# Performance work log

Hardware: AMD Instinct MI355X
Metric: run time of the kernel (lower is better)

## Reference

```python
import jax, jax.numpy as jnp
import numpy as np

N0, N1, N2 = 100000, 50000, 25000
E0, E1 = 400000, 200000
H1, D1 = 4, 64   # layer0: 4 heads x 64
H2, D2 = 1, 64   # layer1: 1 head  x 64
SLOPE = 0.2      # DGL GATConv leaky_relu negative_slope


def gat_conv(h_src, h_dst, src, dst, W, attn_l, attn_r, bias, n_dst, heads, d):
    # linear projection (shared between src and dst, as in DGL GATConv)
    f_src = (h_src @ W).reshape(-1, heads, d)   # (N_src, H, D)
    f_dst = (h_dst @ W).reshape(-1, heads, d)   # (N_dst, H, D)
    el = jnp.einsum('nhd,hd->nh', f_src, attn_l)  # (N_src, H)
    er = jnp.einsum('nhd,hd->nh', f_dst, attn_r)  # (N_dst, H)
    e = jax.nn.leaky_relu(el[src] + er[dst], SLOPE)  # (E, H)
    # edge-softmax over incoming edges of each dst node (numerically stable)
    m = jax.ops.segment_max(e, dst, num_segments=n_dst)      # (N_dst, H)
    ee = jnp.exp(e - m[dst])
    s = jax.ops.segment_sum(ee, dst, num_segments=n_dst)
    alpha = ee / s[dst]                                      # (E, H)
    msg = f_src[src] * alpha[:, :, None]                     # (E, H, D)
    out = jax.ops.segment_sum(msg, dst, num_segments=n_dst)  # (N_dst, H, D)
    return out + bias.reshape(1, heads, d)


def setup_inputs() -> dict:
    key = jax.random.key(0)
    ks = jax.random.split(key, 12)
    return {
        'x': jax.random.normal(ks[0], (N0, 256), jnp.float32),
        'e0_src': jax.random.randint(ks[1], (E0,), 0, N0, jnp.int32),
        'e0_dst': jax.random.randint(ks[2], (E0,), 0, N1, jnp.int32),
        'e1_src': jax.random.randint(ks[3], (E1,), 0, N1, jnp.int32),
        'e1_dst': jax.random.randint(ks[4], (E1,), 0, N2, jnp.int32),
        'W1': jax.random.normal(ks[5], (256, H1 * D1), jnp.float32) * 0.06,
        'al1': jax.random.normal(ks[6], (H1, D1), jnp.float32) * 0.1,
        'ar1': jax.random.normal(ks[7], (H1, D1), jnp.float32) * 0.1,
        'b1': jnp.zeros((H1 * D1,), jnp.float32),
        'W2': jax.random.normal(ks[8], (H1 * D1, H2 * D2), jnp.float32) * 0.06,
        'al2': jax.random.normal(ks[9], (H2, D2), jnp.float32) * 0.1,
        'ar2': jax.random.normal(ks[10], (H2, D2), jnp.float32) * 0.1,
        'b2': jnp.zeros((H2 * D2,), jnp.float32),
    }


def reference(x, e0_src, e0_dst, e1_src, e1_dst,
              W1, al1, ar1, b1, W2, al2, ar2, b2):
    # layer 0: block 100k src -> 50k dst; dst nodes are a prefix of src nodes
    h = gat_conv(x, x[:N1], e0_src, e0_dst, W1, al1, ar1, b1, N1, H1, D1)
    h = jax.nn.relu(h).reshape(N1, H1 * D1)   # activation + flatten(1); dropout is identity at eval
    # layer 1 (final): single head, no activation, flatten
    h = gat_conv(h, h[:N2], e1_src, e1_dst, W2, al2, ar2, b2, N2, H2, D2)
    return h.reshape(N2, H2 * D2)
```

## Files before the change

kernel.cpp:

```cpp
#include <hip/hip_runtime.h>
#include <cstddef>
#include <cstdint>

constexpr int cN0 = 100000, cN1 = 50000, cN2 = 25000;
constexpr int cE0 = 400000, cE1 = 200000;
constexpr float SLOPE = 0.2f;

typedef short short8  __attribute__((ext_vector_type(8)));
typedef short short4v __attribute__((ext_vector_type(4)));
typedef float f32x4   __attribute__((ext_vector_type(4)));

__device__ __forceinline__ unsigned short f2bf(float x) {
    union { float f; uint32_t u; } c; c.f = x;
    uint32_t u = c.u + 0x7FFFu + ((c.u >> 16) & 1u);
    return (unsigned short)(u >> 16);
}
__device__ __forceinline__ float bf2f(uint32_t u) {
    union { uint32_t u; float f; } c; c.u = u << 16; return c.f;
}
__device__ __forceinline__ float lrelu(float x) { return x >= 0.f ? x : SLOPE * x; }


__global__ void hist2_kernel(const int* __restrict__ d0, const int* __restrict__ d1,
                             int* __restrict__ cnt0, int* __restrict__ cnt1) {
    int i = blockIdx.x * blockDim.x + threadIdx.x;
    if (i < cE0) atomicAdd(&cnt0[d0[i]], 1);
    int j = i - cE0;
    if (j >= 0 && j < cE1) atomicAdd(&cnt1[d1[j]], 1);
}

__global__ __launch_bounds__(256) void chunk_sum2_kernel(const int* __restrict__ cnt0, int n0,
                                                         const int* __restrict__ cnt1, int n1,
                                                         int* __restrict__ bsum0, int* __restrict__ bsum1,
                                                         int nblk1) {
    const int* cnt = blockIdx.y ? cnt1 : cnt0;
    int n = blockIdx.y ? n1 : n0;
    int* bsum = blockIdx.y ? bsum1 : bsum0;
    if (blockIdx.y && (int)blockIdx.x >= nblk1) return;
    int i = blockIdx.x * 256 + threadIdx.x;
    int v = (i < n) ? cnt[i] : 0;
    #pragma unroll
    for (int o = 32; o; o >>= 1) v += __shfl_xor(v, o);
    __shared__ int ws[4];
    if ((threadIdx.x & 63) == 0) ws[threadIdx.x >> 6] = v;
    __syncthreads();
    if (threadIdx.x == 0) bsum[blockIdx.x] = ws[0] + ws[1] + ws[2] + ws[3];
}

__device__ __forceinline__ int block_exscan(int v, int& total) {
    int lane = threadIdx.x & 63, w = threadIdx.x >> 6;
    int x = v;
    #pragma unroll
    for (int o = 1; o < 64; o <<= 1) { int t = __shfl_up(x, o); if (lane >= o) x += t; }
    __shared__ int ws[4];
    if (lane == 63) ws[w] = x;
    __syncthreads();
    int add = 0;
    #pragma unroll
    for (int i = 0; i < 4; ++i) if (i < w) add += ws[i];
    total = ws[0] + ws[1] + ws[2] + ws[3];
    return add + x - v;
}

__global__ __launch_bounds__(256) void top_scan2_kernel(const int* __restrict__ bsum0, int nblk0,
                                                        const int* __restrict__ bsum1, int nblk1,
                                                        int* __restrict__ boff0, int* __restrict__ boff1,
                                                        int* __restrict__ tot0, int* __restrict__ tot1) {
    int i = threadIdx.x;
    int tot;
    int v = (i < nblk0) ? bsum0[i] : 0;
    int e = block_exscan(v, tot);
    if (i < nblk0) boff0[i] = e;
    if (i == 0) *tot0 = tot;
    __syncthreads();
    v = (i < nblk1) ? bsum1[i] : 0;
    e = block_exscan(v, tot);
    if (i < nblk1) boff1[i] = e;
    if (i == 0) *tot1 = tot;
}

__global__ __launch_bounds__(256) void chunk_scan2_kernel(const int* __restrict__ cnt0, int n0,
                                                          const int* __restrict__ cnt1, int n1,
                                                          const int* __restrict__ boff0, const int* __restrict__ boff1,
                                                          int* __restrict__ offs0, int* __restrict__ cursor0,
                                                          int* __restrict__ offs1, int* __restrict__ cursor1,
                                                          int nblk1) {
    const int* cnt = blockIdx.y ? cnt1 : cnt0;
    const int* boff = blockIdx.y ? boff1 : boff0;
    int* offs = blockIdx.y ? offs1 : offs0;
    int* cursor = blockIdx.y ? cursor1 : cursor0;
    int n = blockIdx.y ? n1 : n0;
    if (blockIdx.y && (int)blockIdx.x >= nblk1) return;
    int i = blockIdx.x * 256 + threadIdx.x;
    int v = (i < n) ? cnt[i] : 0;
    int tot; int e = block_exscan(v, tot) + boff[blockIdx.x];
    if (i < n) { offs[i] = e; cursor[i] = e; }
}

__global__ void scatter2_kernel(const int* __restrict__ s0, const int* __restrict__ d0,
                                const int* __restrict__ s1, const int* __restrict__ d1,
                                int* __restrict__ cursor0, int* __restrict__ srcidx0,
                                int* __restrict__ cursor1, int* __restrict__ srcidx1) {
    int i = blockIdx.x * blockDim.x + threadIdx.x;
    if (i < cE0) { int p = atomicAdd(&cursor0[d0[i]], 1); srcidx0[p] = s0[i]; }
    int j = i - cE0;
    if (j >= 0 && j < cE1) { int p = atomicAdd(&cursor1[d1[j]], 1); srcidx1[p] = s1[j]; }
}

__global__ __launch_bounds__(256) void bf16_transpose2_kernel(const float* __restrict__ W1,
                                                              const float* __restrict__ W2,
                                                              short* __restrict__ bt1,
                                                              short* __restrict__ bt2) {
    int i = blockIdx.x * 256 + threadIdx.x;
    if (i < 256 * 256) {
        int k = i >> 8, n = i & 255;
        bt1[(size_t)n * 256 + k] = (short)f2bf(W1[i]);
    } else {
        int j = i - 256 * 256;
        if (j < 256 * 64) {
            int k = j >> 6, n = j & 63;
            bt2[(size_t)n * 256 + k] = (short)f2bf(W2[j]);
        }
    }
}

__global__ __launch_bounds__(512, 4) void gemm0_deep(
    const float* __restrict__ A, const short* __restrict__ BT,
    unsigned short* __restrict__ C,
    const float* __restrict__ al, const float* __restrict__ ar,
    float* __restrict__ el, float* __restrict__ er,
    int M, int K, int erN)
{
    constexpr int BM = 128, BN = 256, BK = 32;
    constexpr int PITCH = BK + 8;
    constexpr int WR = 2, WC = 4;
    constexpr int MI = BM / WR / 16;
    constexpr int NI = BN / WC / 16;
    constexpr int nh = 4;

    __shared__ short As[2][BM * PITCH];
    __shared__ short Bs[2][BN * PITCH];

    const int tid = threadIdx.x;
    const int w = tid >> 6;
    const int lane = tid & 63;
    const int ln = lane & 15;
    const int kg = lane >> 4;
    const int wr = w / WC;
    const int wc = w % WC;
    const int m0 = blockIdx.x * BM;
    const int N = BN;

    f32x4 acc[MI][NI];
    #pragma unroll
    for (int mi = 0; mi < MI; ++mi)
        #pragma unroll
        for (int ni = 0; ni < NI; ++ni)
            #pragma unroll
            for (int j = 0; j < 4; ++j) acc[mi][ni][j] = 0.f;

    float4 areg[2];
    short8 breg[2];

    auto loadA = [&](int k0) {
        #pragma unroll
        for (int p = 0; p < 2; ++p) {
            int slot = tid + p * 512;
            int r = slot >> 3;
            int kq = (slot & 7) * 4;
            int gr = m0 + r;
            float4 v = make_float4(0.f, 0.f, 0.f, 0.f);
            if (gr < M) v = *(const float4*)&A[(size_t)gr * K + k0 + kq];
            areg[p] = v;
        }
    };
    auto loadB = [&](int k0) {
        #pragma unroll
        for (int p = 0; p < 2; ++p) {
            int slot = tid + p * 512;
            int r = slot >> 2;
            int kq = (slot & 3) * 8;
            breg[p] = *(const short8*)&BT[(size_t)r * K + k0 + kq];
        }
    };
    auto writeLDS = [&](int c) {
        #pragma unroll
        for (int p = 0; p < 2; ++p) {
            int slot = tid + p * 512;
            int r = slot >> 3;
            int kq = (slot & 7) * 4;
            short4v s;
            s[0] = (short)f2bf(areg[p].x); s[1] = (short)f2bf(areg[p].y);
            s[2] = (short)f2bf(areg[p].z); s[3] = (short)f2bf(areg[p].w);
            *(short4v*)&As[c][r * PITCH + kq] = s;
        }
        #pragma unroll
        for (int p = 0; p < 2; ++p) {
            int slot = tid + p * 512;
            int r = slot >> 2;
            int kq = (slot & 3) * 8;
            *(short8*)&Bs[c][r * PITCH + kq] = breg[p];
        }
    };

    loadA(0); loadB(0);
    writeLDS(0);
    __syncthreads();

    const int T = K / BK;
    int cur = 0;
    for (int t = 0; t < T; ++t) {
        if (t + 1 < T) { loadA((t + 1) * BK); loadB((t + 1) * BK); }
        short8 af[MI];
        #pragma unroll
        for (int mi = 0; mi < MI; ++mi)
            af[mi] = *(const short8*)&As[cur][(wr * MI * 16 + mi * 16 + ln) * PITCH + kg * 8];
        #pragma unroll
        for (int ni = 0; ni < NI; ++ni) {
            short8 bf = *(const short8*)&Bs[cur][(wc * NI * 16 + ni * 16 + ln) * PITCH + kg * 8];
            #pragma unroll
            for (int mi = 0; mi < MI; ++mi)
                acc[mi][ni] = __builtin_amdgcn_mfma_f32_16x16x32_bf16(af[mi], bf, acc[mi][ni], 0, 0, 0);
        }
        if (t + 1 < T) { writeLDS(cur ^ 1); cur ^= 1; }
        __syncthreads();
    }

    const int h = wc;
    float alv[NI], arv[NI];
    #pragma unroll
    for (int ni = 0; ni < NI; ++ni) {
        alv[ni] = al[h * 64 + ni * 16 + ln];
        arv[ni] = ar[h * 64 + ni * 16 + ln];
    }
    #pragma unroll
    for (int mi = 0; mi < MI; ++mi) {
        float pl[4] = {0, 0, 0, 0}, pr[4] = {0, 0, 0, 0};
        #pragma unroll
        for (int ni = 0; ni < NI; ++ni)
            #pragma unroll
            for (int j = 0; j < 4; ++j) {
                float v = acc[mi][ni][j];
                pl[j] += v * alv[ni];
                pr[j] += v * arv[ni];
            }
        #pragma unroll
        for (int j = 0; j < 4; ++j)
            #pragma unroll
            for (int o = 1; o < 16; o <<= 1) {
                pl[j] += __shfl_xor(pl[j], o);
                pr[j] += __shfl_xor(pr[j], o);
            }
        #pragma unroll
        for (int j = 0; j < 4; ++j) {
            int row = m0 + wr * MI * 16 + mi * 16 + kg * 4 + j;
            if (row < M) {
                #pragma unroll
                for (int ni = 0; ni < NI; ++ni)
                    C[(size_t)row * N + wc * 64 + ni * 16 + ln] = f2bf(acc[mi][ni][j]);
                if (ln == 0) {
                    el[row * nh + h] = pl[j];
                    if (row < erN) er[row * nh + h] = pr[j];
                }
            }
        }
    }
}

template<int BM, int BN, int WR, int WC>
__global__ __launch_bounds__(256) void gemm_bf16_fused(
    const unsigned short* __restrict__ A, const short* __restrict__ BT,
    unsigned short* __restrict__ C,
    const float* __restrict__ al, const float* __restrict__ ar,
    float* __restrict__ el, float* __restrict__ er,
    int M, int K, int nh, int erN)
{
    constexpr int BK = 32;
    constexpr int PITCH = BK + 8;
    constexpr int MI = BM / WR / 16;
    constexpr int NI = BN / WC / 16;
    constexpr int AITB = BM * 4 / 256;
    constexpr int BIT  = BN * 4 / 256;

    __shared__ short As[BM * PITCH];
    __shared__ short Bs[BN * PITCH];

    const int tid = threadIdx.x;
    const int w = tid >> 6;
    const int lane = tid & 63;
    const int ln = lane & 15;
    const int kg = lane >> 4;
    const int wr = w / WC;
    const int wc = w % WC;
    const int m0 = blockIdx.x * BM;
    const int n0 = blockIdx.y * BN;
    const int N = nh * 64;

    f32x4 acc[MI][NI];
    #pragma unroll
    for (int mi = 0; mi < MI; ++mi)
        #pragma unroll
        for (int ni = 0; ni < NI; ++ni)
            #pragma unroll
            for (int j = 0; j < 4; ++j) acc[mi][ni][j] = 0.f;

    short8 aregb[AITB];
    short8 breg[BIT];

    auto loadA = [&](int k0) {
        #pragma unroll
        for (int p = 0; p < AITB; ++p) {
            int slot = tid + p * 256;
            int r = slot >> 2;
            int kq = (slot & 3) * 8;
            int gr = m0 + r;
            short8 v = {};
            if (gr < M) v = *(const short8*)&A[(size_t)gr * K + k0 + kq];
            aregb[p] = v;
        }
    };
    auto loadB = [&](int k0) {
        #pragma unroll
        for (int p = 0; p < BIT; ++p) {
            int slot = tid + p * 256;
            int r = slot >> 2;
            int kq = (slot & 3) * 8;
            breg[p] = *(const short8*)&BT[(size_t)(n0 + r) * K + k0 + kq];
        }
    };
    auto writeLDS = [&]() {
        #pragma unroll
        for (int p = 0; p < AITB; ++p) {
            int slot = tid + p * 256;
            int r = slot >> 2;
            int kq = (slot & 3) * 8;
            *(short8*)&As[r * PITCH + kq] = aregb[p];
        }
        #pragma unroll
        for (int p = 0; p < BIT; ++p) {
            int slot = tid + p * 256;
            int r = slot >> 2;
            int kq = (slot & 3) * 8;
            *(short8*)&Bs[r * PITCH + kq] = breg[p];
        }
    };

    loadA(0); loadB(0);
    const int T = K / BK;
    for (int t = 0; t < T; ++t) {
        writeLDS();
        __syncthreads();
        if (t + 1 < T) { loadA((t + 1) * BK); loadB((t + 1) * BK); }
        short8 af[MI], bf[NI];
        #pragma unroll
        for (int mi = 0; mi < MI; ++mi)
            af[mi] = *(const short8*)&As[(wr * MI * 16 + mi * 16 + ln) * PITCH + kg * 8];
        #pragma unroll
        for (int ni = 0; ni < NI; ++ni)
            bf[ni] = *(const short8*)&Bs[(wc * NI * 16 + ni * 16 + ln) * PITCH + kg * 8];
        #pragma unroll
        for (int mi = 0; mi < MI; ++mi)
            #pragma unroll
            for (int ni = 0; ni < NI; ++ni)
                acc[mi][ni] = __builtin_amdgcn_mfma_f32_16x16x32_bf16(af[mi], bf[ni], acc[mi][ni], 0, 0, 0);
        __syncthreads();
    }

    const int h = (n0 + wc * NI * 16) >> 6;
    float alv[NI], arv[NI];
    #pragma unroll
    for (int ni = 0; ni < NI; ++ni) {
        alv[ni] = al[h * 64 + ni * 16 + ln];
        arv[ni] = ar[h * 64 + ni * 16 + ln];
    }
    #pragma unroll
    for (int mi = 0; mi < MI; ++mi) {
        float pl[4] = {0, 0, 0, 0}, pr[4] = {0, 0, 0, 0};
        #pragma unroll
        for (int ni = 0; ni < NI; ++ni)
            #pragma unroll
            for (int j = 0; j < 4; ++j) {
                float v = acc[mi][ni][j];
                pl[j] += v * alv[ni];
                pr[j] += v * arv[ni];
            }
        #pragma unroll
        for (int j = 0; j < 4; ++j)
            #pragma unroll
            for (int o = 1; o < 16; o <<= 1) {
                pl[j] += __shfl_xor(pl[j], o);
                pr[j] += __shfl_xor(pr[j], o);
            }
        #pragma unroll
        for (int j = 0; j < 4; ++j) {
            int row = m0 + wr * MI * 16 + mi * 16 + kg * 4 + j;
            if (row < M) {
                #pragma unroll
                for (int ni = 0; ni < NI; ++ni)
                    C[(size_t)row * N + n0 + wc * NI * 16 + ni * 16 + ln] = f2bf(acc[mi][ni][j]);
                if (ln == 0) {
                    el[row * nh + h] = pl[j];
                    if (row < erN) er[row * nh + h] = pr[j];
                }
            }
        }
    }
}


__global__ __launch_bounds__(256) void agg0_kernel(const int* __restrict__ offs,
                                                   const int* __restrict__ srcidx,
                                                   const float* __restrict__ el,
                                                   const float* __restrict__ er,
                                                   const unsigned short* __restrict__ fb,
                                                   const float* __restrict__ bias,
                                                   unsigned short* __restrict__ h1b) {
    int w = threadIdx.x >> 6, lane = threadIdx.x & 63;
    int n = blockIdx.x * 4 + w;
    if (n >= cN1) return;
    int beg = offs[n], end = offs[n + 1];

    int h4 = lane & 3, sub = lane >> 2;
    float erA = er[n * 4 + h4];
    float m = -1e30f, s = 0.f;
    for (int i = beg + sub; i < end; i += 16) {
        int sv = srcidx[i];
        float e = lrelu(el[sv * 4 + h4] + erA);
        if (e > m) { s = s * __expf(m - e) + 1.f; m = e; }
        else s += __expf(e - m);
    }
    #pragma unroll
    for (int o = 4; o < 64; o <<= 1) {
        float m2 = __shfl_xor(m, o), s2 = __shfl_xor(s, o);
        float M = fmaxf(m, m2);
        s = s * __expf(m - M) + s2 * __expf(m2 - M);
        m = M;
    }
    float inv = (s > 0.f) ? 1.f / s : 0.f;

    int half = lane >> 5, lcol = lane & 31;
    int hB = lcol >> 3;
    float mB = __shfl(m, hB);
    float invB = __shfl(inv, hB);
    float erB = __shfl(erA, hB);

    float a[8] = {};
    for (int i = beg + half; i < end; i += 2) {
        int sv = srcidx[i];
        float e = lrelu(el[sv * 4 + hB] + erB);
        float p = __expf(e - mB) * invB;
        uint4 v = *(const uint4*)&fb[(size_t)sv * 256 + lcol * 8];
        a[0] = fmaf(bf2f(v.x & 0xffffu), p, a[0]);
        a[1] = fmaf(bf2f(v.x >> 16),     p, a[1]);
        a[2] = fmaf(bf2f(v.y & 0xffffu), p, a[2]);
        a[3] = fmaf(bf2f(v.y >> 16),     p, a[3]);
        a[4] = fmaf(bf2f(v.z & 0xffffu), p, a[4]);
        a[5] = fmaf(bf2f(v.z >> 16),     p, a[5]);
        a[6] = fmaf(bf2f(v.w & 0xffffu), p, a[6]);
        a[7] = fmaf(bf2f(v.w >> 16),     p, a[7]);
    }
    #pragma unroll
    for (int j = 0; j < 8; ++j) a[j] += __shfl_xor(a[j], 32);
    if (half == 0) {
        short8 r;
        #pragma unroll
        for (int j = 0; j < 8; ++j) {
            float o = a[j] + bias[lcol * 8 + j];
            r[j] = (short)f2bf(o > 0.f ? o : 0.f);
        }
        *(short8*)&h1b[(size_t)n * 256 + lcol * 8] = r;
    }
}

__global__ __launch_bounds__(256) void agg1_kernel(const int* __restrict__ offs,
                                                   const int* __restrict__ srcidx,
                                                   const float* __restrict__ el,
                                                   const float* __restrict__ er,
                                                   const unsigned short* __restrict__ f2b,
                                                   const float* __restrict__ bias,
                                                   float* __restrict__ out) {
    int w = threadIdx.x >> 6, lane = threadIdx.x & 63;
    int n = blockIdx.x * 4 + w;
    if (n >= cN2) return;
    int beg = offs[n], end = offs[n + 1];
    float ern = er[n];

    float m = -1e30f, s = 0.f;
    for (int i = beg + lane; i < end; i += 64) {
        float e = lrelu(el[srcidx[i]] + ern);
        if (e > m) { s = s * __expf(m - e) + 1.f; m = e; }
        else s += __expf(e - m);
    }
    #pragma unroll
    for (int o = 1; o < 64; o <<= 1) {
        float m2 = __shfl_xor(m, o), s2 = __shfl_xor(s, o);
        float M = fmaxf(m, m2);
        s = s * __expf(m - M) + s2 * __expf(m2 - M);
        m = M;
    }
    float inv = (s > 0.f) ? 1.f / s : 0.f;

    int q = lane >> 4, lcol = lane & 15;
    float a[4] = {};
    for (int i = beg + q; i < end; i += 4) {
        int sv = srcidx[i];
        float e = lrelu(el[sv] + ern);
        float p = __expf(e - m) * inv;
        uint2 v = *(const uint2*)&f2b[(size_t)sv * 64 + lcol * 4];
        a[0] = fmaf(bf2f(v.x & 0xffffu), p, a[0]);
        a[1] = fmaf(bf2f(v.x >> 16),     p, a[1]);
        a[2] = fmaf(bf2f(v.y & 0xffffu), p, a[2]);
        a[3] = fmaf(bf2f(v.y >> 16),     p, a[3]);
    }
    #pragma unroll
    for (int o = 16; o < 64; o <<= 1)
        #pragma unroll
        for (int j = 0; j < 4; ++j) a[j] += __shfl_xor(a[j], o);
    if (q == 0) {
        float4 b4 = *(const float4*)&bias[lcol * 4];
        float4 r = make_float4(a[0] + b4.x, a[1] + b4.y, a[2] + b4.z, a[3] + b4.w);
        *(float4*)&out[(size_t)n * 64 + lcol * 4] = r;
    }
}


extern "C" void kernel_launch(void* const* d_in, const int* in_sizes, int n_in,
                              void* d_out, int out_size, void* d_ws, size_t ws_size,
                              hipStream_t stream) {
    const float* x      = (const float*)d_in[0];
    const int*   e0_src = (const int*)d_in[1];
    const int*   e0_dst = (const int*)d_in[2];
    const int*   e1_src = (const int*)d_in[3];
    const int*   e1_dst = (const int*)d_in[4];
    const float* W1     = (const float*)d_in[5];
    const float* al1    = (const float*)d_in[6];
    const float* ar1    = (const float*)d_in[7];
    const float* b1     = (const float*)d_in[8];
    const float* W2     = (const float*)d_in[9];
    const float* al2    = (const float*)d_in[10];
    const float* ar2    = (const float*)d_in[11];
    const float* b2     = (const float*)d_in[12];
    float* out = (float*)d_out;

    char* ws = (char*)d_ws;
    size_t off = 0;
    auto alloc = [&](size_t bytes) -> void* {
        void* p = ws + off;
        off = (off + bytes + 255) & ~(size_t)255;
        return p;
    };
    unsigned short* fb  = (unsigned short*)alloc((size_t)cN0 * 256 * 2);
    unsigned short* h1b = (unsigned short*)alloc((size_t)cN1 * 256 * 2);
    unsigned short* f2b = (unsigned short*)alloc((size_t)cN1 * 64 * 2);
    float* el0  = (float*)alloc((size_t)cN0 * 4 * 4);
    float* er0  = (float*)alloc((size_t)cN1 * 4 * 4);
    float* el2  = (float*)alloc((size_t)cN1 * 4);
    float* er2  = (float*)alloc((size_t)cN2 * 4);
    short* bt1  = (short*)alloc((size_t)256 * 256 * 2);
    short* bt2  = (short*)alloc((size_t)64 * 256 * 2);
    int* cntB    = (int*)alloc((size_t)(cN1 + cN2) * 4);
    int* cnt0    = cntB;
    int* cnt1    = cntB + cN1;
    int* offs0   = (int*)alloc((size_t)(cN1 + 1) * 4);
    int* cursor0 = (int*)alloc((size_t)cN1 * 4);
    int* srcidx0 = (int*)alloc((size_t)cE0 * 4);
    int* offs1   = (int*)alloc((size_t)(cN2 + 1) * 4);
    int* cursor1 = (int*)alloc((size_t)cN2 * 4);
    int* srcidx1 = (int*)alloc((size_t)cE1 * 4);
    int* bsum0   = (int*)alloc(256 * 4);
    int* boff0   = (int*)alloc(256 * 4);
    int* bsum1   = (int*)alloc(256 * 4);
    int* boff1   = (int*)alloc(256 * 4);
    (void)ws_size; (void)n_in; (void)in_sizes; (void)out_size;

    const int nblk0 = (cN1 + 255) / 256;
    const int nblk1 = (cN2 + 255) / 256;

    hipMemsetAsync(cntB, 0, (size_t)(cN1 + cN2) * 4, stream);
    hist2_kernel<<<(cE0 + cE1 + 255) / 256, 256, 0, stream>>>(e0_dst, e1_dst, cnt0, cnt1);
    chunk_sum2_kernel<<<dim3(nblk0, 2), 256, 0, stream>>>(cnt0, cN1, cnt1, cN2, bsum0, bsum1, nblk1);
    top_scan2_kernel<<<1, 256, 0, stream>>>(bsum0, nblk0, bsum1, nblk1, boff0, boff1,
                                            offs0 + cN1, offs1 + cN2);
    chunk_scan2_kernel<<<dim3(nblk0, 2), 256, 0, stream>>>(cnt0, cN1, cnt1, cN2, boff0, boff1,
                                                           offs0, cursor0, offs1, cursor1, nblk1);
    scatter2_kernel<<<(cE0 + cE1 + 255) / 256, 256, 0, stream>>>(e0_src, e0_dst, e1_src, e1_dst,
                                                                 cursor0, srcidx0, cursor1, srcidx1);
    bf16_transpose2_kernel<<<(256 * 256 + 256 * 64 + 255) / 256, 256, 0, stream>>>(W1, W2, bt1, bt2);

    gemm0_deep<<<(cN0 + 127) / 128, 512, 0, stream>>>(x, bt1, fb, al1, ar1, el0, er0, cN0, 256, cN1);
    agg0_kernel<<<(cN1 + 3) / 4, 256, 0, stream>>>(offs0, srcidx0, el0, er0, fb, b1, h1b);

    gemm_bf16_fused<128, 64, 4, 1><<<dim3((cN1 + 127) / 128, 1), 256, 0, stream>>>(
        h1b, bt2, f2b, al2, ar2, el2, er2, cN1, 256, 1, cN2);
    agg1_kernel<<<(cN2 + 3) / 4, 256, 0, stream>>>(offs1, srcidx1, el2, er2, f2b, b2, out);
}
```

Before: 186.4 us.

## Stage layer-0 GEMM tiles with direct global-to-LDS loads and XOR swizzle

Rewrites the first projection GEMM so that A (fp32) and B tiles go straight from global memory into LDS through global_load_lds, with no detour through registers. The LDS tiles use an XOR swizzle instead of padding, and A stays fp32 in LDS and is converted to bf16 at fragment-read time with packed v_cvt_pk_bf16_f32. K is fixed at 256 and the k-loop is fully unrolled. The aim is to cut register pressure and the VALU conversion and store work in the staging path. The cost is a larger fp32 A tile in LDS, which may lower occupancy, and correctness that depends on the swizzle layout matching the buffer-load LDS placement.

```diff
diff --git a/kernel.cpp b/kernel.cpp
--- a/kernel.cpp
+++ b/kernel.cpp
@@ -19,6 +19,18 @@
     union { uint32_t u; float f; } c; c.u = u << 16; return c.f;
 }
 __device__ __forceinline__ float lrelu(float x) { return x >= 0.f ? x : SLOPE * x; }
+
+__device__ __forceinline__ uint32_t cvtpk(float lo, float hi) {
+    uint32_t r;
+    asm("v_cvt_pk_bf16_f32 %0, %1, %2" : "=v"(r) : "v"(lo), "v"(hi));
+    return r;
+}
+
+__device__ __forceinline__ void gload_lds16(const void* g, void* l) {
+    __builtin_amdgcn_global_load_lds(
+        (const __attribute__((address_space(1))) unsigned int*)g,
+        (__attribute__((address_space(3))) unsigned int*)l, 16, 0, 0);
+}
 
 
 __global__ void hist2_kernel(const int* __restrict__ d0, const int* __restrict__ d1,
@@ -129,115 +141,102 @@
     unsigned short* __restrict__ C,
     const float* __restrict__ al, const float* __restrict__ ar,
     float* __restrict__ el, float* __restrict__ er,
-    int M, int K, int erN)
+    int M, int erN)
 {
-    constexpr int BM = 128, BN = 256, BK = 32;
-    constexpr int PITCH = BK + 8;
-    constexpr int WR = 2, WC = 4;
-    constexpr int MI = BM / WR / 16;
-    constexpr int NI = BN / WC / 16;
+    constexpr int T = 8;
     constexpr int nh = 4;
-
-    __shared__ short As[2][BM * PITCH];
-    __shared__ short Bs[2][BN * PITCH];
+    __shared__ float Asm[2][128 * 32];
+    __shared__ short Bsm[2][256 * 32];
 
     const int tid = threadIdx.x;
     const int w = tid >> 6;
     const int lane = tid & 63;
     const int ln = lane & 15;
     const int kg = lane >> 4;
-    const int wr = w / WC;
-    const int wc = w % WC;
-    const int m0 = blockIdx.x * BM;
-    const int N = BN;
-
-    f32x4 acc[MI][NI];
-    #pragma unroll
-    for (int mi = 0; mi < MI; ++mi)
-        #pragma unroll
-        for (int ni = 0; ni < NI; ++ni)
+    const int wr = w >> 2;
+    const int wc = w & 3;
+    const int m0 = blockIdx.x * 128;
+
+    f32x4 acc[4][4];
+    #pragma unroll
+    for (int mi = 0; mi < 4; ++mi)
+        #pragma unroll
+        for (int ni = 0; ni < 4; ++ni)
             #pragma unroll
             for (int j = 0; j < 4; ++j) acc[mi][ni][j] = 0.f;
 
-    float4 areg[2];
-    short8 breg[2];
-
-    auto loadA = [&](int k0) {
-        #pragma unroll
-        for (int p = 0; p < 2; ++p) {
-            int slot = tid + p * 512;
-            int r = slot >> 3;
-            int kq = (slot & 7) * 4;
-            int gr = m0 + r;
-            float4 v = make_float4(0.f, 0.f, 0.f, 0.f);
-            if (gr < M) v = *(const float4*)&A[(size_t)gr * K + k0 + kq];
-            areg[p] = v;
+    auto stageA = [&](int k0, int b) {
+        #pragma unroll
+        for (int q = 0; q < 2; ++q) {
+            int ci = w + q * 8;
+            int r = ci * 8 + (lane >> 3);
+            int cl = (lane & 7) ^ (r & 7);
+            int gr = m0 + r; if (gr >= M) gr = M - 1;
+            gload_lds16(&A[(size_t)gr * 256 + k0 + cl * 4], &Asm[b][ci * 256]);
         }
     };
-    auto loadB = [&](int k0) {
-        #pragma unroll
-        for (int p = 0; p < 2; ++p) {
-            int slot = tid + p * 512;
-            int r = slot >> 2;
-            int kq = (slot & 3) * 8;
-            breg[p] = *(const short8*)&BT[(size_t)r * K + k0 + kq];
+    auto stageB = [&](int k0, int b) {
+        #pragma unroll
+        for (int q = 0; q < 2; ++q) {
+            int ci = w + q * 8;
+            int r = ci * 16 + (lane >> 2);
+            int cl = (lane & 3) ^ ((r >> 1) & 3);
+            gload_lds16(&BT[(size_t)r * 256 + k0 + cl * 8], &Bsm[b][ci * 512]);
         }
     };
-    auto writeLDS = [&](int c) {
-        #pragma unroll
-        for (int p = 0; p < 2; ++p) {
-            int slot = tid + p * 512;
-            int r = slot >> 3;
-            int kq = (slot & 7) * 4;
-            short4v s;
-            s[0] = (short)f2bf(areg[p].x); s[1] = (short)f2bf(areg[p].y);
-            s[2] = (short)f2bf(areg[p].z); s[3] = (short)f2bf(areg[p].w);
-            *(short4v*)&As[c][r * PITCH + kq] = s;
-        }
-        #pragma unroll
-        for (int p = 0; p < 2; ++p) {
-            int slot = tid + p * 512;
-            int r = slot >> 2;
-            int kq = (slot & 3) * 8;
-            *(short8*)&Bs[c][r * PITCH + kq] = breg[p];
-        }
-    };
-
-    loadA(0); loadB(0);
-    writeLDS(0);
+
+    stageA(0, 0); stageB(0, 0);
     __syncthreads();
 
-    const int T = K / BK;
+    const int swa = ln & 7;
+    const int p0base = 2 * kg;
+    const int pb = kg ^ ((ln >> 1) & 3);
+
     int cur = 0;
+    #pragma unroll
     for (int t = 0; t < T; ++t) {
-        if (t + 1 < T) { loadA((t + 1) * BK); loadB((t + 1) * BK); }
-        short8 af[MI];
-        #pragma unroll
-        for (int mi = 0; mi < MI; ++mi)
-            af[mi] = *(const short8*)&As[cur][(wr * MI * 16 + mi * 16 + ln) * PITCH + kg * 8];
-        #pragma unroll
-        for (int ni = 0; ni < NI; ++ni) {
-            short8 bf = *(const short8*)&Bs[cur][(wc * NI * 16 + ni * 16 + ln) * PITCH + kg * 8];
-            #pragma unroll
-            for (int mi = 0; mi < MI; ++mi)
+        if (t + 1 < T) { stageA((t + 1) * 32, cur ^ 1); stageB((t + 1) * 32, cur ^ 1); }
+
+        short8 af[4];
+        {
+            int pA = p0base ^ swa;
+            #pragma unroll
+            for (int mi = 0; mi < 4; ++mi) {
+                int r = wr * 64 + mi * 16 + ln;
+                const f32x4 q0 = *(const f32x4*)&Asm[cur][r * 32 + pA * 4];
+                const f32x4 q1 = *(const f32x4*)&Asm[cur][r * 32 + (pA ^ 1) * 4];
+                union { uint32_t u[4]; short8 s; } cv;
+                cv.u[0] = cvtpk(q0[0], q0[1]);
+                cv.u[1] = cvtpk(q0[2], q0[3]);
+                cv.u[2] = cvtpk(q1[0], q1[1]);
+                cv.u[3] = cvtpk(q1[2], q1[3]);
+                af[mi] = cv.s;
+            }
+        }
+        #pragma unroll
+        for (int ni = 0; ni < 4; ++ni) {
+            int rB = wc * 64 + ni * 16 + ln;
+            short8 bf = *(const short8*)&Bsm[cur][rB * 32 + pb * 8];
+            #pragma unroll
+            for (int mi = 0; mi < 4; ++mi)
                 acc[mi][ni] = __builtin_amdgcn_mfma_f32_16x16x32_bf16(af[mi], bf, acc[mi][ni], 0, 0, 0);
         }
-        if (t + 1 < T) { writeLDS(cur ^ 1); cur ^= 1; }
         __syncthreads();
+        cur ^= 1;
     }
 
     const int h = wc;
-    float alv[NI], arv[NI];
-    #pragma unroll
-    for (int ni = 0; ni < NI; ++ni) {
+    float alv[4], arv[4];
+    #pragma unroll
+    for (int ni = 0; ni < 4; ++ni) {
         alv[ni] = al[h * 64 + ni * 16 + ln];
         arv[ni] = ar[h * 64 + ni * 16 + ln];
     }
     #pragma unroll
-    for (int mi = 0; mi < MI; ++mi) {
+    for (int mi = 0; mi < 4; ++mi) {
         float pl[4] = {0, 0, 0, 0}, pr[4] = {0, 0, 0, 0};
         #pragma unroll
-        for (int ni = 0; ni < NI; ++ni)
+        for (int ni = 0; ni < 4; ++ni)
             #pragma unroll
             for (int j = 0; j < 4; ++j) {
                 float v = acc[mi][ni][j];
@@ -253,11 +252,11 @@
             }
         #pragma unroll
         for (int j = 0; j < 4; ++j) {
-            int row = m0 + wr * MI * 16 + mi * 16 + kg * 4 + j;
+            int row = m0 + wr * 64 + mi * 16 + kg * 4 + j;
             if (row < M) {
                 #pragma unroll
-                for (int ni = 0; ni < NI; ++ni)
-                    C[(size_t)row * N + wc * 64 + ni * 16 + ln] = f2bf(acc[mi][ni][j]);
+                for (int ni = 0; ni < 4; ++ni)
+                    C[(size_t)row * 256 + wc * 64 + ni * 16 + ln] = f2bf(acc[mi][ni][j]);
                 if (ln == 0) {
                     el[row * nh + h] = pl[j];
                     if (row < erN) er[row * nh + h] = pr[j];
@@ -587,7 +586,7 @@
                                                                  cursor0, srcidx0, cursor1, srcidx1);
     bf16_transpose2_kernel<<<(256 * 256 + 256 * 64 + 255) / 256, 256, 0, stream>>>(W1, W2, bt1, bt2);
 
-    gemm0_deep<<<(cN0 + 127) / 128, 512, 0, stream>>>(x, bt1, fb, al1, ar1, el0, er0, cN0, 256, cN1);
+    gemm0_deep<<<(cN0 + 127) / 128, 512, 0, stream>>>(x, bt1, fb, al1, ar1, el0, er0, cN0, cN1);
     agg0_kernel<<<(cN1 + 3) / 4, 256, 0, stream>>>(offs0, srcidx0, el0, er0, fb, b1, h1b);
 
     gemm_bf16_fused<128, 64, 4, 1><<<dim3((cN1 + 127) / 128, 1), 256, 0, stream>>>(
```

Result: no change. 184.3 us (-1.1%).
